# Kernel optimization log

Measured on AMD Instinct MI355X. Metric: run time of the kernel, lower is better.

Reference implementation:

```python
import jax, jax.numpy as jnp
import numpy as np

H = 1024
V = 32000
L = 15
B = 512


def setup_inputs() -> dict:
    key = jax.random.key(0)
    ks = jax.random.split(key, 16)
    s = 0.02
    return {
        "input_ids": jax.random.randint(ks[0], (B,), 0, V),
        "hidden": jax.random.normal(ks[1], (1, B, H), jnp.float32),
        "encoder_outputs": jax.random.normal(ks[2], (L, B, H), jnp.float32),
        "max_length": L,
        "embedding": jax.random.normal(ks[3], (V, H), jnp.float32) * s,
        "attn1_w": jax.random.normal(ks[4], (1, 2 * H), jnp.float32) * s,
        "attn1_b": jnp.zeros((1,), jnp.float32),
        "combine_w": jax.random.normal(ks[5], (H, 2 * H), jnp.float32) * s,
        "combine_b": jnp.zeros((H,), jnp.float32),
        "w_ih": jax.random.normal(ks[6], (3 * H, H), jnp.float32) * s,
        "w_hh": jax.random.normal(ks[7], (3 * H, H), jnp.float32) * s,
        "b_ih": jnp.zeros((3 * H,), jnp.float32),
        "b_hh": jnp.zeros((3 * H,), jnp.float32),
        "out_w": jax.random.normal(ks[8], (V, H), jnp.float32) * s,
        "out_b": jnp.zeros((V,), jnp.float32),
    }


def reference(input_ids, hidden, encoder_outputs, max_length, embedding,
              attn1_w, attn1_b, combine_w, combine_b,
              w_ih, w_hh, b_ih, b_hh, out_w, out_b):
    # embedding lookup (dropout is identity in eval mode)
    emb = embedding[input_ids]                       # [B, H]
    # Bahdanau-style additive scores: vectorize the per-step python loop
    emb_l = jnp.broadcast_to(emb[None], (max_length, B, H))   # [L, B, H]
    cat = jnp.concatenate([emb_l, encoder_outputs], axis=-1)  # [L, B, 2H]
    scores = cat @ attn1_w.T + attn1_b               # [L, B, 1]
    attn_weights = jax.nn.softmax(scores, axis=0)    # softmax over L
    ctx = jnp.sum(attn_weights * encoder_outputs, axis=0)     # [B, H]
    x = jnp.concatenate([emb, ctx], axis=-1) @ combine_w.T + combine_b  # [B, H]
    # n_layers = 1: relu then one GRU step (seq len 1)
    x = jax.nn.relu(x)
    h = hidden[0]                                    # [B, H]
    gi = x @ w_ih.T + b_ih                           # [B, 3H]
    gh = h @ w_hh.T + b_hh                           # [B, 3H]
    i_r, i_z, i_n = jnp.split(gi, 3, axis=1)
    h_r, h_z, h_n = jnp.split(gh, 3, axis=1)
    r = jax.nn.sigmoid(i_r + h_r)
    z = jax.nn.sigmoid(i_z + h_z)
    n = jnp.tanh(i_n + r * h_n)
    h_new = (1.0 - z) * n + z * h                    # [B, H]
    logits = h_new @ out_w.T + out_b                 # [B, V]
    output = jax.nn.log_softmax(logits, axis=1)
    return output, h_new[None], attn_weights
```

## Files before the change

kernel.cpp:

```cpp
#include <hip/hip_runtime.h>

#define HH 1024
#define VV 32000
#define LL 15
#define BB 512

typedef __bf16 bf16;
typedef __bf16 bf16x4 __attribute__((ext_vector_type(4)));
typedef __bf16 bf16x8 __attribute__((ext_vector_type(8)));
typedef float f32x4 __attribute__((ext_vector_type(4)));

#define VMCNT(n) asm volatile("s_waitcnt vmcnt(" #n ")" ::: "memory")
#define SBAR     __builtin_amdgcn_s_barrier()
#define SCHED0   __builtin_amdgcn_sched_barrier(0)

__device__ __forceinline__ unsigned short f2bf(float f) {
    unsigned int u = __float_as_uint(f);
    unsigned int r = (u + 0x7fffu + ((u >> 16) & 1u)) >> 16;
    return (unsigned short)r;
}
__device__ __forceinline__ float bf2f(unsigned short u) {
    return __uint_as_float(((unsigned int)u) << 16);
}

__device__ __forceinline__ void gld_lds16(const void* g, void* l) {
    __builtin_amdgcn_global_load_lds(
        (const __attribute__((address_space(1))) unsigned int*)g,
        (__attribute__((address_space(3))) unsigned int*)l, 16, 0, 0);
}

#define PACKU  (VV * HH / 8)
#define CVT0   (3 * HH * HH / 8)
#define CVT1   (3 * HH * HH / 8)
#define CVT2   (2 * HH * HH / 8)
#define CVT3   (BB * HH / 8)
#define TOTALU (PACKU + CVT0 + CVT1 + CVT2 + CVT3)

__global__ __launch_bounds__(256)
void stream_kernel(const float* __restrict__ out_w, unsigned short* __restrict__ packed,
                   const float* __restrict__ w_ih, unsigned short* __restrict__ w_ih_bf,
                   const float* __restrict__ w_hh, unsigned short* __restrict__ w_hh_bf,
                   const float* __restrict__ combine_w, unsigned short* __restrict__ w_cb_bf,
                   const float* __restrict__ hidden, unsigned short* __restrict__ hid_bf) {
    const int stride = gridDim.x * 256;
    for (int u = blockIdx.x * 256 + threadIdx.x; u < TOTALU; u += stride) {
        if (u < PACKU) {
            const int g  = u >> 14;
            const int dd = u & 16383;
            const int kt = dd >> 10;
            const int ot = dd & 1023;
            const int rl = ot >> 3;
            const int ko = (ot & 7) * 8;
            const float* src = out_w + ((size_t)(g * 128 + rl)) * 1024 + kt * 64 + ko;
            const f32x4 a = *(const f32x4*)src;
            const f32x4 b = *(const f32x4*)(src + 4);
            bf16x8 w;
            const bf16x4 wa = __builtin_convertvector(a, bf16x4);
            const bf16x4 wb = __builtin_convertvector(b, bf16x4);
            #pragma unroll
            for (int c = 0; c < 4; c++) { w[c] = wa[c]; w[c + 4] = wb[c]; }
            *(bf16x8*)&packed[(size_t)u * 8] = w;
        } else {
            int i = u - PACKU;
            const float* src; unsigned short* dst;
            if (i < CVT0) { src = w_ih; dst = w_ih_bf; }
            else if ((i -= CVT0) < CVT1) { src = w_hh; dst = w_hh_bf; }
            else if ((i -= CVT1) < CVT2) { src = combine_w; dst = w_cb_bf; }
            else { i -= CVT2; src = hidden; dst = hid_bf; }
            const f32x4 a = ((const f32x4*)src)[2 * i];
            const f32x4 b = ((const f32x4*)src)[2 * i + 1];
            bf16x8 w;
            const bf16x4 wa = __builtin_convertvector(a, bf16x4);
            const bf16x4 wb = __builtin_convertvector(b, bf16x4);
            #pragma unroll
            for (int c = 0; c < 4; c++) { w[c] = wa[c]; w[c + 4] = wb[c]; }
            *(bf16x8*)&dst[(size_t)i * 8] = w;
        }
    }
}

__global__ __launch_bounds__(256)
void attn_kernel(const int* __restrict__ ids, const float* __restrict__ enc,
                 const float* __restrict__ embedding,
                 const float* __restrict__ attn1_w, const float* __restrict__ attn1_b,
                 float* __restrict__ attn_out, unsigned short* __restrict__ cat_out) {
    const int b = blockIdx.x, tid = threadIdx.x;
    const int lane = tid & 63, wv = tid >> 6;

    __shared__ float s_enc[LL * HH];
    __shared__ float s_scores[LL];
    __shared__ float s_red[4];

    for (int idx = tid; idx < LL * HH / 4; idx += 256) {
        const int l = (idx * 4) >> 10, h = (idx * 4) & (HH - 1);
        *(f32x4*)&s_enc[idx * 4] = *(const f32x4*)&enc[((size_t)l * BB + b) * HH + h];
    }

    const float* embr = embedding + (size_t)ids[b] * HH;
    float p = 0.f;
    for (int j = tid; j < HH; j += 256) p += embr[j] * attn1_w[j];
    #pragma unroll
    for (int o = 32; o; o >>= 1) p += __shfl_xor(p, o);
    if (lane == 0) s_red[wv] = p;
    __syncthreads();
    const float semb = s_red[0] + s_red[1] + s_red[2] + s_red[3] + attn1_b[0];

    for (int l = wv; l < LL; l += 4) {
        float q = 0.f;
        for (int j = lane; j < HH; j += 64) q += s_enc[l * HH + j] * attn1_w[HH + j];
        #pragma unroll
        for (int o = 32; o; o >>= 1) q += __shfl_xor(q, o);
        if (lane == 0) s_scores[l] = q + semb;
    }
    __syncthreads();

    float mx = -3.4e38f;
    #pragma unroll
    for (int l = 0; l < LL; l++) mx = fmaxf(mx, s_scores[l]);
    float aw[LL], sum = 0.f;
    #pragma unroll
    for (int l = 0; l < LL; l++) { aw[l] = __expf(s_scores[l] - mx); sum += aw[l]; }
    const float inv = 1.f / sum;
    #pragma unroll
    for (int l = 0; l < LL; l++) aw[l] *= inv;

    if (tid < LL) attn_out[tid * BB + b] = aw[tid];

    for (int j = tid; j < HH; j += 256) {
        float c = 0.f;
        #pragma unroll
        for (int l = 0; l < LL; l++) c += aw[l] * s_enc[l * HH + j];
        cat_out[(size_t)b * (2 * HH) + j] = f2bf(embr[j]);
        cat_out[(size_t)b * (2 * HH) + HH + j] = f2bf(c);
    }
}

template<int TM, int TN, int OUT, int GATES>
__global__ __launch_bounds__(256)
void gemm_nt(const bf16* __restrict__ A, const bf16* __restrict__ B,
             const float* __restrict__ bias, void* __restrict__ Cout,
             const bf16* __restrict__ A2, const bf16* __restrict__ B2,
             const float* __restrict__ bias2, void* __restrict__ C2,
             const int K, const int N) {
    constexpr int FM = TM / 32, FN = TN / 32;
    __shared__ bf16 As[2][TM * 64];
    __shared__ bf16 Bs[2][TN * 64];

    if (GATES && blockIdx.z == 1) { A = A2; B = B2; bias = bias2; Cout = C2; }

    const int tid = threadIdx.x;
    const int lane = tid & 63, wave = tid >> 6;
    const int wm = wave >> 1, wn = wave & 1;
    const int rlo = lane & 15, khi = lane >> 4;
    const int m0 = blockIdx.y * TM, n0 = blockIdx.x * TN;

    f32x4 acc[FM][FN] = {};
    constexpr int IA = TM / 32, IB = TN / 32;

    auto stage = [&](int k0, int buf) {
        #pragma unroll
        for (int i = 0; i < IA; i++) {
            const int p = (i * 256 + tid) * 16;
            const int row = p >> 7;
            const int qs = (p & 127) ^ ((row & 7) << 4);
            gld_lds16(A + (size_t)(m0 + row) * K + k0 + (qs >> 1),
                      &As[buf][0] + i * 2048 + wave * 512);
        }
        #pragma unroll
        for (int i = 0; i < IB; i++) {
            const int p = (i * 256 + tid) * 16;
            const int row = p >> 7;
            const int qs = (p & 127) ^ ((row & 7) << 4);
            gld_lds16(B + (size_t)(n0 + row) * K + k0 + (qs >> 1),
                      &Bs[buf][0] + i * 2048 + wave * 512);
        }
    };

    auto compute = [&](int buf) {
        #pragma unroll
        for (int ks = 0; ks < 2; ks++) {
            bf16x8 af[FM], bfr[FN];
            #pragma unroll
            for (int m = 0; m < FM; m++) {
                const int r = wm * (TM / 2) + m * 16 + rlo;
                const int sw = (ks * 64 + khi * 16) ^ ((r & 7) << 4);
                af[m] = *(const bf16x8*)((const char*)&As[buf][0] + r * 128 + sw);
            }
            #pragma unroll
            for (int n = 0; n < FN; n++) {
                const int r = wn * (TN / 2) + n * 16 + rlo;
                const int sw = (ks * 64 + khi * 16) ^ ((r & 7) << 4);
                bfr[n] = *(const bf16x8*)((const char*)&Bs[buf][0] + r * 128 + sw);
            }
            #pragma unroll
            for (int m = 0; m < FM; m++)
                #pragma unroll
                for (int n = 0; n < FN; n++)
                    acc[m][n] = __builtin_amdgcn_mfma_f32_16x16x32_bf16(af[m], bfr[n], acc[m][n], 0, 0, 0);
        }
    };

    const int NT = K >> 6;
    stage(0, 0);
    stage(64, 1);

    for (int kt = 0; kt < NT; kt += 2) {
        {
            const int t = kt;
            if (t + 1 < NT) { VMCNT(4); } else { VMCNT(0); }
            SCHED0; SBAR; SCHED0;
            compute(0);
            SCHED0; SBAR; SCHED0;
            if (t + 2 < NT) stage((t + 2) << 6, 0);
        }
        {
            const int t = kt + 1;
            if (t + 1 < NT) { VMCNT(4); } else { VMCNT(0); }
            SCHED0; SBAR; SCHED0;
            compute(1);
            SCHED0; SBAR; SCHED0;
            if (t + 2 < NT) stage((t + 2) << 6, 1);
        }
    }

    #pragma unroll
    for (int m = 0; m < FM; m++) {
        const int gr = m0 + wm * (TM / 2) + m * 16 + khi * 4;
        #pragma unroll
        for (int n = 0; n < FN; n++) {
            const int gc = n0 + wn * (TN / 2) + n * 16 + rlo;
            const float bv = bias[gc];
            #pragma unroll
            for (int j = 0; j < 4; j++) {
                float v = acc[m][n][j] + bv;
                if (OUT == 1) {
                    v = fmaxf(v, 0.f);
                    ((unsigned short*)Cout)[(size_t)(gr + j) * N + gc] = f2bf(v);
                } else {
                    ((float*)Cout)[(size_t)(gr + j) * N + gc] = v;
                }
            }
        }
    }
}

template<int CB>
__global__ __launch_bounds__(256, 2)
void gemm_out(const bf16* __restrict__ A, const bf16* __restrict__ Bp,
              const float* __restrict__ bias, float* __restrict__ C,
              unsigned short* __restrict__ Cb,
              float* __restrict__ pmax, float* __restrict__ psum) {
    constexpr int K = HH, N = VV;
    __shared__ bf16 As[2][128 * 64];
    __shared__ bf16 Bs[2][128 * 64];
    __shared__ float sPm[2][128], sPs[2][128];

    const int tid = threadIdx.x;
    const int lane = tid & 63, wave = tid >> 6;
    const int wm = wave >> 1, wn = wave & 1;
    const int rlo = lane & 15, khi = lane >> 4;

    constexpr int gridN = 250;
    constexpr int nFull = (gridN >> 3) << 5;
    const int bidx = blockIdx.x;
    int g, jm;
    if (bidx < nFull) { const int s = bidx >> 5, rem = bidx & 31; jm = rem >> 3; g = s * 8 + (rem & 7); }
    else { const int rem = bidx - nFull; constexpr int gleft = gridN & 7; g = (gridN & ~7) + rem % gleft; jm = rem / gleft; }
    const int n0 = g * 128, m0 = jm * 128;

    const char* pb = (const char*)(Bp + (size_t)g * 131072);

    f32x4 acc[4][4] = {};

    auto stage = [&](int k0, int buf) {
        #pragma unroll
        for (int i = 0; i < 4; i++) {
            const int p = (i * 256 + tid) * 16;
            const int row = p >> 7;
            const int qs = (p & 127) ^ ((row & 7) << 4);
            gld_lds16(A + (size_t)(m0 + row) * K + k0 + (qs >> 1),
                      &As[buf][0] + i * 2048 + wave * 512);
        }
        #pragma unroll
        for (int i = 0; i < 4; i++) {
            const int p = (i * 256 + tid) * 16;
            const int row = p >> 7;
            const int qs = (p & 127) ^ ((row & 7) << 4);
            gld_lds16(pb + (size_t)(k0 >> 6) * 16384 + row * 128 + qs,
                      &Bs[buf][0] + i * 2048 + wave * 512);
        }
    };

    auto compute = [&](int buf) {
        #pragma unroll
        for (int ks = 0; ks < 2; ks++) {
            bf16x8 af[4], bfr[4];
            #pragma unroll
            for (int m = 0; m < 4; m++) {
                const int r = wm * 64 + m * 16 + rlo;
                const int sw = (ks * 64 + khi * 16) ^ ((r & 7) << 4);
                af[m] = *(const bf16x8*)((const char*)&As[buf][0] + r * 128 + sw);
            }
            #pragma unroll
            for (int n = 0; n < 4; n++) {
                const int r = wn * 64 + n * 16 + rlo;
                const int sw = (ks * 64 + khi * 16) ^ ((r & 7) << 4);
                bfr[n] = *(const bf16x8*)((const char*)&Bs[buf][0] + r * 128 + sw);
            }
            #pragma unroll
            for (int m = 0; m < 4; m++)
                #pragma unroll
                for (int n = 0; n < 4; n++)
                    acc[m][n] = __builtin_amdgcn_mfma_f32_16x16x32_bf16(af[m], bfr[n], acc[m][n], 0, 0, 0);
        }
    };

    constexpr int NT = K >> 6;
    stage(0, 0);
    stage(64, 1);

    for (int kt = 0; kt < NT; kt += 2) {
        {
            const int t = kt;
            if (t + 1 < NT) { VMCNT(8); } else { VMCNT(0); }
            SCHED0; SBAR; SCHED0;
            compute(0);
            SCHED0; SBAR; SCHED0;
            if (t + 2 < NT) stage((t + 2) << 6, 0);
        }
        {
            const int t = kt + 1;
            if (t + 1 < NT) { VMCNT(8); } else { VMCNT(0); }
            SCHED0; SBAR; SCHED0;
            compute(1);
            SCHED0; SBAR; SCHED0;
            if (t + 2 < NT) stage((t + 2) << 6, 1);
        }
    }

    float bvn[4];
    #pragma unroll
    for (int n = 0; n < 4; n++) bvn[n] = bias[n0 + wn * 64 + n * 16 + rlo];

    #pragma unroll
    for (int m = 0; m < 4; m++) {
        const int rbase = wm * 64 + m * 16 + khi * 4;
        #pragma unroll
        for (int j = 0; j < 4; j++) {
            const int gr = m0 + rbase + j;
            float v[4];
            float lm = -3.4e38f;
            #pragma unroll
            for (int n = 0; n < 4; n++) {
                v[n] = acc[m][n][j] + bvn[n];
                const size_t ci = (size_t)gr * N + n0 + wn * 64 + n * 16 + rlo;
                if (CB) Cb[ci] = f2bf(v[n]); else C[ci] = v[n];
                lm = fmaxf(lm, v[n]);
            }
            #pragma unroll
            for (int o = 8; o; o >>= 1) lm = fmaxf(lm, __shfl_xor(lm, o));
            float ls = 0.f;
            #pragma unroll
            for (int n = 0; n < 4; n++) ls += __expf(v[n] - lm);
            #pragma unroll
            for (int o = 8; o; o >>= 1) ls += __shfl_xor(ls, o);
            if (rlo == 0) { sPm[wn][rbase + j] = lm; sPs[wn][rbase + j] = ls; }
        }
    }
    __syncthreads();
    if (tid < 128) {
        const float ma = sPm[0][tid], mb = sPm[1][tid];
        const float M = fmaxf(ma, mb);
        const float S = sPs[0][tid] * __expf(ma - M) + sPs[1][tid] * __expf(mb - M);
        pmax[(size_t)(m0 + tid) * 256 + g] = M;
        psum[(size_t)(m0 + tid) * 256 + g] = S;
    }
}

__global__ __launch_bounds__(256)
void gru_kernel(const float* __restrict__ gi, const float* __restrict__ gh,
                const float* __restrict__ h, float* __restrict__ hnew,
                unsigned short* __restrict__ hnew_bf) {
    const int i = blockIdx.x * 256 + threadIdx.x;
    const int e = i * 4;
    const int b = e >> 10, j = e & (HH - 1);
    const size_t o = ((size_t)b * 3 * HH + j) / 4;
    const f32x4 ir = ((const f32x4*)gi)[o],          iz = ((const f32x4*)gi)[o + HH / 4],
                in_ = ((const f32x4*)gi)[o + 2 * HH / 4];
    const f32x4 hr = ((const f32x4*)gh)[o],          hz = ((const f32x4*)gh)[o + HH / 4],
                hn = ((const f32x4*)gh)[o + 2 * HH / 4];
    const f32x4 hv = ((const f32x4*)h)[i];
    f32x4 out;
    ushort4 ob;
    #pragma unroll
    for (int c = 0; c < 4; c++) {
        const float r = 1.f / (1.f + __expf(-(ir[c] + hr[c])));
        const float z = 1.f / (1.f + __expf(-(iz[c] + hz[c])));
        const float n = tanhf(in_[c] + r * hn[c]);
        const float v = (1.f - z) * n + z * hv[c];
        out[c] = v;
        ((unsigned short*)&ob)[c] = f2bf(v);
    }
    ((f32x4*)hnew)[i] = out;
    ((ushort4*)hnew_bf)[i] = ob;
}

template<int CB>
__global__ __launch_bounds__(512)
void lsm_final(const float* __restrict__ pmax, const float* __restrict__ psum,
               const unsigned short* __restrict__ Cb, float* __restrict__ logits) {
    const int b = blockIdx.x, tid = threadIdx.x;
    const int lane = tid & 63, wv = tid >> 6;
    __shared__ float sm[8], ss[8];

    float m = -3.4e38f, s = 0.f;
    if (tid < 250) { m = pmax[(size_t)b * 256 + tid]; s = psum[(size_t)b * 256 + tid]; }
    #pragma unroll
    for (int o = 32; o; o >>= 1) {
        const float mo = __shfl_xor(m, o), so = __shfl_xor(s, o);
        const float nm = fmaxf(m, mo);
        s = s * __expf(m - nm) + so * __expf(mo - nm);
        m = nm;
    }
    if (lane == 0) { sm[wv] = m; ss[wv] = s; }
    __syncthreads();
    float M = sm[0], S;
    #pragma unroll
    for (int w = 1; w < 8; w++) M = fmaxf(M, sm[w]);
    S = ss[0] * __expf(sm[0] - M);
    #pragma unroll
    for (int w = 1; w < 8; w++) S += ss[w] * __expf(sm[w] - M);
    const float lse = M + __logf(S);

    float* row = logits + (size_t)b * VV;
    if (CB) {
        const unsigned short* rowc = Cb + (size_t)b * VV;
        for (int j = tid; j < VV / 8; j += 512) {
            const ushort4 u0 = ((const ushort4*)rowc)[2 * j];
            const ushort4 u1 = ((const ushort4*)rowc)[2 * j + 1];
            f32x4 v0, v1;
            v0[0] = bf2f(u0.x) - lse; v0[1] = bf2f(u0.y) - lse;
            v0[2] = bf2f(u0.z) - lse; v0[3] = bf2f(u0.w) - lse;
            v1[0] = bf2f(u1.x) - lse; v1[1] = bf2f(u1.y) - lse;
            v1[2] = bf2f(u1.z) - lse; v1[3] = bf2f(u1.w) - lse;
            ((f32x4*)row)[2 * j] = v0;
            ((f32x4*)row)[2 * j + 1] = v1;
        }
    } else {
        for (int j = tid; j < VV / 4; j += 512) {
            f32x4 v = ((const f32x4*)row)[j];
            v[0] -= lse; v[1] -= lse; v[2] -= lse; v[3] -= lse;
            ((f32x4*)row)[j] = v;
        }
    }
}

extern "C" void kernel_launch(void* const* d_in, const int* in_sizes, int n_in,
                              void* d_out, int out_size, void* d_ws, size_t ws_size,
                              hipStream_t stream) {
    const int*   ids       = (const int*)d_in[0];
    const float* hidden    = (const float*)d_in[1];
    const float* enc       = (const float*)d_in[2];
    const float* embedding = (const float*)d_in[4];
    const float* attn1_w   = (const float*)d_in[5];
    const float* attn1_b   = (const float*)d_in[6];
    const float* combine_w = (const float*)d_in[7];
    const float* combine_b = (const float*)d_in[8];
    const float* w_ih      = (const float*)d_in[9];
    const float* w_hh      = (const float*)d_in[10];
    const float* b_ih      = (const float*)d_in[11];
    const float* b_hh      = (const float*)d_in[12];
    const float* out_w     = (const float*)d_in[13];
    const float* out_b     = (const float*)d_in[14];

    float* out_lsm = (float*)d_out;
    float* out_h   = out_lsm + (size_t)BB * VV;
    float* out_aw  = out_h + (size_t)BB * HH;

    char* w = (char*)d_ws;
    unsigned short* packed   = (unsigned short*)w;   w += (size_t)VV * HH * 2;
    unsigned short* w_ih_bf  = (unsigned short*)w;   w += (size_t)3 * HH * HH * 2;
    unsigned short* w_hh_bf  = (unsigned short*)w;   w += (size_t)3 * HH * HH * 2;
    unsigned short* w_cb_bf  = (unsigned short*)w;   w += (size_t)2 * HH * HH * 2;
    unsigned short* cat_bf   = (unsigned short*)w;   w += (size_t)BB * 2 * HH * 2;
    unsigned short* x_bf     = (unsigned short*)w;   w += (size_t)BB * HH * 2;
    unsigned short* hid_bf   = (unsigned short*)w;   w += (size_t)BB * HH * 2;
    unsigned short* hnew_bf  = (unsigned short*)w;   w += (size_t)BB * HH * 2;
    float* gi   = (float*)w;                         w += (size_t)BB * 3 * HH * 4;
    float* gh   = (float*)w;                         w += (size_t)BB * 3 * HH * 4;
    float* pmax = (float*)w;                         w += (size_t)BB * 256 * 4;
    float* psum = (float*)w;                         w += (size_t)BB * 256 * 4;
    unsigned short* Cb = (unsigned short*)w;
    const size_t needed_cb = (size_t)(w - (char*)d_ws) + (size_t)BB * VV * 2;
    const bool use_cb = ws_size >= needed_cb;

    stream_kernel<<<2048, 256, 0, stream>>>(
        out_w, packed, w_ih, w_ih_bf, w_hh, w_hh_bf, combine_w, w_cb_bf, hidden, hid_bf);

    attn_kernel<<<BB, 256, 0, stream>>>(ids, enc, embedding, attn1_w, attn1_b, out_aw, cat_bf);

    gemm_nt<64, 64, 1, 0><<<dim3(HH / 64, BB / 64), 256, 0, stream>>>(
        (const bf16*)cat_bf, (const bf16*)w_cb_bf, combine_b, x_bf,
        nullptr, nullptr, nullptr, nullptr, 2 * HH, HH);

    gemm_nt<64, 64, 0, 1><<<dim3(3 * HH / 64, BB / 64, 2), 256, 0, stream>>>(
        (const bf16*)hid_bf, (const bf16*)w_hh_bf, b_hh, gh,
        (const bf16*)x_bf, (const bf16*)w_ih_bf, b_ih, gi, HH, 3 * HH);

    gru_kernel<<<(BB * HH / 4) / 256, 256, 0, stream>>>(gi, gh, hidden, out_h, hnew_bf);

    if (use_cb) {
        gemm_out<1><<<1000, 256, 0, stream>>>(
            (const bf16*)hnew_bf, (const bf16*)packed, out_b, nullptr, Cb, pmax, psum);
        lsm_final<1><<<BB, 512, 0, stream>>>(pmax, psum, Cb, out_lsm);
    } else {
        gemm_out<0><<<1000, 256, 0, stream>>>(
            (const bf16*)hnew_bf, (const bf16*)packed, out_b, out_lsm, nullptr, pmax, psum);
        lsm_final<0><<<BB, 512, 0, stream>>>(pmax, psum, nullptr, out_lsm);
    }
}
```

Measured before the change: 179.3 us.

## Read fp32 out_w directly in output GEMM, drop bf16 pre-pack pass

The separate pass that converted and repacked the 32000x1024 fp32 output weight into bf16 is removed. The output GEMM now stages fp32 weight tiles straight into LDS, with an XOR swizzle, and converts them to bf16 in registers before the MFMA. A loads directly from global memory. The tile becomes 256x64 with 512 threads, and the partial max/sum arrays grow to 500 column groups, which lsm_final now reads. This avoids one full read and write of the weight, at the cost of a single-buffered, unpipelined K loop and per-use conversion work.

```diff
diff --git a/kernel.cpp b/kernel.cpp
--- a/kernel.cpp
+++ b/kernel.cpp
@@ -29,53 +29,34 @@
         (__attribute__((address_space(3))) unsigned int*)l, 16, 0, 0);
 }
 
-#define PACKU  (VV * HH / 8)
 #define CVT0   (3 * HH * HH / 8)
 #define CVT1   (3 * HH * HH / 8)
 #define CVT2   (2 * HH * HH / 8)
-#define CVT3   (BB * HH / 8)
-#define TOTALU (PACKU + CVT0 + CVT1 + CVT2 + CVT3)
+#define NCVTB  544
 
 __global__ __launch_bounds__(256)
-void stream_kernel(const float* __restrict__ out_w, unsigned short* __restrict__ packed,
-                   const float* __restrict__ w_ih, unsigned short* __restrict__ w_ih_bf,
-                   const float* __restrict__ w_hh, unsigned short* __restrict__ w_hh_bf,
-                   const float* __restrict__ combine_w, unsigned short* __restrict__ w_cb_bf,
-                   const float* __restrict__ hidden, unsigned short* __restrict__ hid_bf) {
-    const int stride = gridDim.x * 256;
-    for (int u = blockIdx.x * 256 + threadIdx.x; u < TOTALU; u += stride) {
-        if (u < PACKU) {
-            const int g  = u >> 14;
-            const int dd = u & 16383;
-            const int kt = dd >> 10;
-            const int ot = dd & 1023;
-            const int rl = ot >> 3;
-            const int ko = (ot & 7) * 8;
-            const float* src = out_w + ((size_t)(g * 128 + rl)) * 1024 + kt * 64 + ko;
-            const f32x4 a = *(const f32x4*)src;
-            const f32x4 b = *(const f32x4*)(src + 4);
-            bf16x8 w;
-            const bf16x4 wa = __builtin_convertvector(a, bf16x4);
-            const bf16x4 wb = __builtin_convertvector(b, bf16x4);
-            #pragma unroll
-            for (int c = 0; c < 4; c++) { w[c] = wa[c]; w[c + 4] = wb[c]; }
-            *(bf16x8*)&packed[(size_t)u * 8] = w;
-        } else {
-            int i = u - PACKU;
-            const float* src; unsigned short* dst;
-            if (i < CVT0) { src = w_ih; dst = w_ih_bf; }
-            else if ((i -= CVT0) < CVT1) { src = w_hh; dst = w_hh_bf; }
-            else if ((i -= CVT1) < CVT2) { src = combine_w; dst = w_cb_bf; }
-            else { i -= CVT2; src = hidden; dst = hid_bf; }
-            const f32x4 a = ((const f32x4*)src)[2 * i];
-            const f32x4 b = ((const f32x4*)src)[2 * i + 1];
-            bf16x8 w;
-            const bf16x4 wa = __builtin_convertvector(a, bf16x4);
-            const bf16x4 wb = __builtin_convertvector(b, bf16x4);
-            #pragma unroll
-            for (int c = 0; c < 4; c++) { w[c] = wa[c]; w[c + 4] = wb[c]; }
-            *(bf16x8*)&dst[(size_t)i * 8] = w;
-        }
+void cvt_kernel(const float* __restrict__ w_ih, unsigned short* __restrict__ w_ih_bf,
+                const float* __restrict__ w_hh, unsigned short* __restrict__ w_hh_bf,
+                const float* __restrict__ combine_w, unsigned short* __restrict__ w_cb_bf,
+                const float* __restrict__ hidden, unsigned short* __restrict__ hid_bf) {
+    int ub = blockIdx.x * 2048 + threadIdx.x;
+    const float* src; unsigned short* dst;
+    if (ub < CVT0) { src = w_ih; dst = w_ih_bf; }
+    else if ((ub -= CVT0) < CVT1) { src = w_hh; dst = w_hh_bf; }
+    else if ((ub -= CVT1) < CVT2) { src = combine_w; dst = w_cb_bf; }
+    else { ub -= CVT2; src = hidden; dst = hid_bf; }
+
+    #pragma unroll
+    for (int q = 0; q < 8; q++) {
+        const int i = ub + q * 256;
+        const f32x4 a = ((const f32x4*)src)[2 * i];
+        const f32x4 b = ((const f32x4*)src)[2 * i + 1];
+        const bf16x4 wa = __builtin_convertvector(a, bf16x4);
+        const bf16x4 wb = __builtin_convertvector(b, bf16x4);
+        bf16x8 w;
+        #pragma unroll
+        for (int c = 0; c < 4; c++) { w[c] = wa[c]; w[c + 4] = wb[c]; }
+        *(bf16x8*)&dst[(size_t)i * 8] = w;
     }
 }
 
@@ -245,102 +226,78 @@
 }
 
 template<int CB>
-__global__ __launch_bounds__(256, 2)
-void gemm_out(const bf16* __restrict__ A, const bf16* __restrict__ Bp,
-              const float* __restrict__ bias, float* __restrict__ C,
-              unsigned short* __restrict__ Cb,
-              float* __restrict__ pmax, float* __restrict__ psum) {
+__global__ __launch_bounds__(512, 2)
+void gemm_direct(const bf16* __restrict__ A, const float* __restrict__ B,
+                 const float* __restrict__ bias, float* __restrict__ C,
+                 unsigned short* __restrict__ Cb,
+                 float* __restrict__ pmax, float* __restrict__ psum) {
     constexpr int K = HH, N = VV;
-    __shared__ bf16 As[2][128 * 64];
-    __shared__ bf16 Bs[2][128 * 64];
-    __shared__ float sPm[2][128], sPs[2][128];
+    __shared__ __align__(16) float Bsf[64 * 256];
+    __shared__ float sPm[2][256], sPs[2][256];
 
     const int tid = threadIdx.x;
     const int lane = tid & 63, wave = tid >> 6;
     const int wm = wave >> 1, wn = wave & 1;
     const int rlo = lane & 15, khi = lane >> 4;
 
-    constexpr int gridN = 250;
-    constexpr int nFull = (gridN >> 3) << 5;
+    constexpr int gridN = 500;
+    constexpr int nFull = (gridN >> 3) << 4;
     const int bidx = blockIdx.x;
     int g, jm;
-    if (bidx < nFull) { const int s = bidx >> 5, rem = bidx & 31; jm = rem >> 3; g = s * 8 + (rem & 7); }
-    else { const int rem = bidx - nFull; constexpr int gleft = gridN & 7; g = (gridN & ~7) + rem % gleft; jm = rem / gleft; }
-    const int n0 = g * 128, m0 = jm * 128;
-
-    const char* pb = (const char*)(Bp + (size_t)g * 131072);
-
-    f32x4 acc[4][4] = {};
-
-    auto stage = [&](int k0, int buf) {
-        #pragma unroll
-        for (int i = 0; i < 4; i++) {
-            const int p = (i * 256 + tid) * 16;
-            const int row = p >> 7;
-            const int qs = (p & 127) ^ ((row & 7) << 4);
-            gld_lds16(A + (size_t)(m0 + row) * K + k0 + (qs >> 1),
-                      &As[buf][0] + i * 2048 + wave * 512);
-        }
-        #pragma unroll
-        for (int i = 0; i < 4; i++) {
-            const int p = (i * 256 + tid) * 16;
-            const int row = p >> 7;
-            const int qs = (p & 127) ^ ((row & 7) << 4);
-            gld_lds16(pb + (size_t)(k0 >> 6) * 16384 + row * 128 + qs,
-                      &Bs[buf][0] + i * 2048 + wave * 512);
-        }
-    };
-
-    auto compute = [&](int buf) {
-        #pragma unroll
-        for (int ks = 0; ks < 2; ks++) {
-            bf16x8 af[4], bfr[4];
-            #pragma unroll
-            for (int m = 0; m < 4; m++) {
-                const int r = wm * 64 + m * 16 + rlo;
-                const int sw = (ks * 64 + khi * 16) ^ ((r & 7) << 4);
-                af[m] = *(const bf16x8*)((const char*)&As[buf][0] + r * 128 + sw);
+    if (bidx < nFull) { const int s = bidx >> 4, rem = bidx & 15; jm = rem >> 3; g = s * 8 + (rem & 7); }
+    else { const int rem = bidx - nFull; g = 496 + (rem & 3); jm = rem >> 2; }
+    const int n0 = g * 64, m0 = jm * 256;
+
+    f32x4 acc[4][2] = {};
+
+    const bf16* Arow = A + (size_t)(m0 + wm * 64 + rlo) * K;
+
+    for (int t = 0; t < 4; t++) {
+        #pragma unroll
+        for (int i = 0; i < 8; i++) {
+            const int r = i * 8 + wave;
+            const int cb = (lane * 16) ^ ((r & 7) << 5);
+            gld_lds16(B + (size_t)(n0 + r) * K + t * 256 + (cb >> 2),
+                      (char*)Bsf + r * 1024);
+        }
+        VMCNT(0);
+        SCHED0; SBAR; SCHED0;
+
+        #pragma unroll
+        for (int kstep = 0; kstep < 4; kstep++) {
+            #pragma unroll
+            for (int ks = 0; ks < 2; ks++) {
+                const int koff = kstep * 64 + ks * 32 + khi * 8;
+                bf16x8 af[4], bfr[2];
+                #pragma unroll
+                for (int m = 0; m < 4; m++)
+                    af[m] = *(const bf16x8*)(Arow + (size_t)m * 16 * K + t * 256 + koff);
+                #pragma unroll
+                for (int n = 0; n < 2; n++) {
+                    const int r = wn * 32 + n * 16 + rlo;
+                    const char* p = (const char*)Bsf + r * 1024 + ((koff * 4) ^ ((r & 7) << 5));
+                    const f32x4 lo = *(const f32x4*)p;
+                    const f32x4 hi = *(const f32x4*)(p + 16);
+                    const bf16x4 wa = __builtin_convertvector(lo, bf16x4);
+                    const bf16x4 wb = __builtin_convertvector(hi, bf16x4);
+                    bf16x8 w;
+                    #pragma unroll
+                    for (int c = 0; c < 4; c++) { w[c] = wa[c]; w[c + 4] = wb[c]; }
+                    bfr[n] = w;
+                }
+                #pragma unroll
+                for (int m = 0; m < 4; m++)
+                    #pragma unroll
+                    for (int n = 0; n < 2; n++)
+                        acc[m][n] = __builtin_amdgcn_mfma_f32_16x16x32_bf16(af[m], bfr[n], acc[m][n], 0, 0, 0);
             }
-            #pragma unroll
-            for (int n = 0; n < 4; n++) {
-                const int r = wn * 64 + n * 16 + rlo;
-                const int sw = (ks * 64 + khi * 16) ^ ((r & 7) << 4);
-                bfr[n] = *(const bf16x8*)((const char*)&Bs[buf][0] + r * 128 + sw);
-            }
-            #pragma unroll
-            for (int m = 0; m < 4; m++)
-                #pragma unroll
-                for (int n = 0; n < 4; n++)
-                    acc[m][n] = __builtin_amdgcn_mfma_f32_16x16x32_bf16(af[m], bfr[n], acc[m][n], 0, 0, 0);
-        }
-    };
-
-    constexpr int NT = K >> 6;
-    stage(0, 0);
-    stage(64, 1);
-
-    for (int kt = 0; kt < NT; kt += 2) {
-        {
-            const int t = kt;
-            if (t + 1 < NT) { VMCNT(8); } else { VMCNT(0); }
-            SCHED0; SBAR; SCHED0;
-            compute(0);
-            SCHED0; SBAR; SCHED0;
-            if (t + 2 < NT) stage((t + 2) << 6, 0);
-        }
-        {
-            const int t = kt + 1;
-            if (t + 1 < NT) { VMCNT(8); } else { VMCNT(0); }
-            SCHED0; SBAR; SCHED0;
-            compute(1);
-            SCHED0; SBAR; SCHED0;
-            if (t + 2 < NT) stage((t + 2) << 6, 1);
-        }
-    }
-
-    float bvn[4];
-    #pragma unroll
-    for (int n = 0; n < 4; n++) bvn[n] = bias[n0 + wn * 64 + n * 16 + rlo];
+        }
+        SCHED0; SBAR; SCHED0;
+    }
+
+    float bvn[2];
+    #pragma unroll
+    for (int n = 0; n < 2; n++) bvn[n] = bias[n0 + wn * 32 + n * 16 + rlo];
 
     #pragma unroll
     for (int m = 0; m < 4; m++) {
@@ -348,32 +305,29 @@
         #pragma unroll
         for (int j = 0; j < 4; j++) {
             const int gr = m0 + rbase + j;
-            float v[4];
-            float lm = -3.4e38f;
-            #pragma unroll
-            for (int n = 0; n < 4; n++) {
+            float v[2];
+            #pragma unroll
+            for (int n = 0; n < 2; n++) {
                 v[n] = acc[m][n][j] + bvn[n];
-                const size_t ci = (size_t)gr * N + n0 + wn * 64 + n * 16 + rlo;
+                const size_t ci = (size_t)gr * N + n0 + wn * 32 + n * 16 + rlo;
                 if (CB) Cb[ci] = f2bf(v[n]); else C[ci] = v[n];
-                lm = fmaxf(lm, v[n]);
             }
+            float lm = fmaxf(v[0], v[1]);
             #pragma unroll
             for (int o = 8; o; o >>= 1) lm = fmaxf(lm, __shfl_xor(lm, o));
-            float ls = 0.f;
-            #pragma unroll
-            for (int n = 0; n < 4; n++) ls += __expf(v[n] - lm);
+            float ls = __expf(v[0] - lm) + __expf(v[1] - lm);
             #pragma unroll
             for (int o = 8; o; o >>= 1) ls += __shfl_xor(ls, o);
             if (rlo == 0) { sPm[wn][rbase + j] = lm; sPs[wn][rbase + j] = ls; }
         }
     }
     __syncthreads();
-    if (tid < 128) {
+    if (tid < 256) {
         const float ma = sPm[0][tid], mb = sPm[1][tid];
         const float M = fmaxf(ma, mb);
         const float S = sPs[0][tid] * __expf(ma - M) + sPs[1][tid] * __expf(mb - M);
-        pmax[(size_t)(m0 + tid) * 256 + g] = M;
-        psum[(size_t)(m0 + tid) * 256 + g] = S;
+        pmax[(size_t)(m0 + tid) * 512 + g] = M;
+        psum[(size_t)(m0 + tid) * 512 + g] = S;
     }
 }
 
@@ -414,7 +368,7 @@
     __shared__ float sm[8], ss[8];
 
     float m = -3.4e38f, s = 0.f;
-    if (tid < 250) { m = pmax[(size_t)b * 256 + tid]; s = psum[(size_t)b * 256 + tid]; }
+    if (tid < 500) { m = pmax[(size_t)b * 512 + tid]; s = psum[(size_t)b * 512 + tid]; }
     #pragma unroll
     for (int o = 32; o; o >>= 1) {
         const float mo = __shfl_xor(m, o), so = __shfl_xor(s, o);
@@ -478,7 +432,6 @@
     float* out_aw  = out_h + (size_t)BB * HH;
 
     char* w = (char*)d_ws;
-    unsigned short* packed   = (unsigned short*)w;   w += (size_t)VV * HH * 2;
     unsigned short* w_ih_bf  = (unsigned short*)w;   w += (size_t)3 * HH * HH * 2;
     unsigned short* w_hh_bf  = (unsigned short*)w;   w += (size_t)3 * HH * HH * 2;
     unsigned short* w_cb_bf  = (unsigned short*)w;   w += (size_t)2 * HH * HH * 2;
@@ -488,14 +441,14 @@
     unsigned short* hnew_bf  = (unsigned short*)w;   w += (size_t)BB * HH * 2;
     float* gi   = (float*)w;                         w += (size_t)BB * 3 * HH * 4;
     float* gh   = (float*)w;                         w += (size_t)BB * 3 * HH * 4;
-    float* pmax = (float*)w;                         w += (size_t)BB * 256 * 4;
-    float* psum = (float*)w;                         w += (size_t)BB * 256 * 4;
+    float* pmax = (float*)w;                         w += (size_t)BB * 512 * 4;
+    float* psum = (float*)w;                         w += (size_t)BB * 512 * 4;
     unsigned short* Cb = (unsigned short*)w;
     const size_t needed_cb = (size_t)(w - (char*)d_ws) + (size_t)BB * VV * 2;
     const bool use_cb = ws_size >= needed_cb;
 
-    stream_kernel<<<2048, 256, 0, stream>>>(
-        out_w, packed, w_ih, w_ih_bf, w_hh, w_hh_bf, combine_w, w_cb_bf, hidden, hid_bf);
+    cvt_kernel<<<NCVTB, 256, 0, stream>>>(
+        w_ih, w_ih_bf, w_hh, w_hh_bf, combine_w, w_cb_bf, hidden, hid_bf);
 
     attn_kernel<<<BB, 256, 0, stream>>>(ids, enc, embedding, attn1_w, attn1_b, out_aw, cat_bf);
 
@@ -510,12 +463,12 @@
     gru_kernel<<<(BB * HH / 4) / 256, 256, 0, stream>>>(gi, gh, hidden, out_h, hnew_bf);
 
     if (use_cb) {
-        gemm_out<1><<<1000, 256, 0, stream>>>(
-            (const bf16*)hnew_bf, (const bf16*)packed, out_b, nullptr, Cb, pmax, psum);
+        gemm_direct<1><<<1000, 512, 0, stream>>>(
+            (const bf16*)hnew_bf, out_w, out_b, nullptr, Cb, pmax, psum);
         lsm_final<1><<<BB, 512, 0, stream>>>(pmax, psum, Cb, out_lsm);
     } else {
-        gemm_out<0><<<1000, 256, 0, stream>>>(
-            (const bf16*)hnew_bf, (const bf16*)packed, out_b, out_lsm, nullptr, pmax, psum);
+        gemm_direct<0><<<1000, 512, 0, stream>>>(
+            (const bf16*)hnew_bf, out_w, out_b, out_lsm, nullptr, pmax, psum);
         lsm_final<0><<<BB, 512, 0, stream>>>(pmax, psum, nullptr, out_lsm);
     }
 }
```

Result: slower. 237.4 us (+32.4%).
